# Kernel tuning notes

Measured on AMD Instinct MI355X. Metric: run time of the kernel, lower is better.

Reference implementation:

```python
import jax, jax.numpy as jnp
import numpy as np

B, D_DATA, D_DICT0, N_SAE, D_DICT = 2048, 768, 128, 128, 32


def _kaiming_uniform(key, shape, fan_in):
    # torch.nn.init.kaiming_uniform_ default: bound = sqrt(6 / fan_in) / sqrt(5-gain stuff) ~ use gain=sqrt(2)? match torch default a=sqrt(5) not needed; plain kaiming_uniform_ uses gain=sqrt(2): bound = sqrt(6/fan_in)*? Keep simple: bound = sqrt(6.0/fan_in)
    bound = np.sqrt(6.0 / fan_in)
    return jax.random.uniform(key, shape, jnp.float32, -bound, bound)


def setup_inputs() -> dict:
    key = jax.random.key(0)
    ks = jax.random.split(key, 6)
    x = jax.random.normal(ks[0], (B, D_DATA), jnp.float32)
    # top-level SAE params
    W_enc0 = _kaiming_uniform(ks[1], (D_DATA, D_DICT0), D_DATA)
    b_enc0 = jnp.zeros((D_DICT0,), jnp.float32)
    W_dec0 = _kaiming_uniform(ks[2], (D_DICT0, D_DATA), D_DICT0)
    W_dec0 = W_dec0 / jnp.linalg.norm(W_dec0, axis=-1, keepdims=True)
    b_dec0 = jnp.zeros((D_DATA,), jnp.float32)
    # sublayer (hierarchical) per-expert params
    W_enc1 = _kaiming_uniform(ks[3], (N_SAE, D_DATA, D_DICT), D_DATA)
    b_enc1 = jnp.zeros((N_SAE, D_DICT), jnp.float32)
    W_dec1 = _kaiming_uniform(ks[4], (N_SAE, D_DICT, D_DATA), D_DICT)
    W_dec1 = W_dec1 / jnp.linalg.norm(W_dec1, axis=-1, keepdims=True)
    b_dec1 = jnp.zeros((N_SAE, D_DATA), jnp.float32)
    return {"x": x, "W_enc0": W_enc0, "b_enc0": b_enc0, "W_dec0": W_dec0,
            "b_dec0": b_dec0, "W_enc1": W_enc1, "b_enc1": b_enc1,
            "W_dec1": W_dec1, "b_dec1": b_dec1}


def reference(x, W_enc0, b_enc0, W_dec0, b_dec0, W_enc1, b_enc1, W_dec1, b_dec1):
    # ---- sae_0 (standard SAE; scale/unscale are identity) ----
    acts0 = jax.nn.relu((x - b_dec0) @ W_enc0 + b_enc0)        # [B, D_DICT0]
    x0 = acts0 @ W_dec0 + b_dec0                               # [B, D_DATA]
    # ---- binary gate over experts (n_sae == d_dict0) ----
    gate = (acts0 > 0).astype(x.dtype)                         # [B, N_SAE]
    # ---- sublayer: gather-encode-decode-scatter, expressed densely with a
    # binary mask (gate only selects membership; gate value is not multiplied).
    # Avoid materializing [B, N_SAE, D_DATA] by distributing (x - b_dec1[j]):
    pre = (jnp.einsum('bd,jdk->bjk', x, W_enc1)
           - jnp.einsum('jd,jdk->jk', b_dec1, W_enc1)[None]
           + b_enc1[None])                                     # [B, N_SAE, D_DICT]
    acts1 = jax.nn.relu(pre) * gate[:, :, None]                # zero out ungated
    # scatter_add over experts: sum_j gated (acts1[b,j] @ W_dec1[j] + b_dec1[j])
    dec = jnp.einsum('bjk,jkd->bd', acts1, W_dec1) + gate @ b_dec1  # [B, D_DATA]
    return x0 + dec
```

## Files before the change

kernel.cpp:

```cpp
#include <hip/hip_runtime.h>
#include <hip/hip_bf16.h>
#include <stdint.h>

#define B_SZ   2048
#define DDATA  768
#define NSAE   128
#define NJK    4096
#define KA2    4352
#define SPLITK 4
#define KC2    1088

typedef unsigned short u16;
typedef short bf16x8 __attribute__((ext_vector_type(8)));
typedef float f32x4  __attribute__((ext_vector_type(4)));

static __device__ __forceinline__ u16 f2bf(float f) {
  __hip_bfloat16 h = __float2bfloat16(f);
  return *reinterpret_cast<u16*>(&h);
}

static __device__ __forceinline__ void gload16(const u16* g, u16* l) {
  __builtin_amdgcn_global_load_lds(
      (const __attribute__((address_space(1))) unsigned int*)g,
      (__attribute__((address_space(3))) unsigned int*)l,
      16, 0, 0);
}

__global__ __launch_bounds__(256) void k_front(const float* __restrict__ x,
                                               const float* __restrict__ We0,
                                               const float* __restrict__ be0,
                                               const float* __restrict__ bd0,
                                               const float* __restrict__ We1,
                                               const float* __restrict__ bd1,
                                               const float* __restrict__ be1,
                                               const float* __restrict__ Wd1,
                                               const float* __restrict__ Wd0,
                                               u16* __restrict__ W1T,
                                               float* __restrict__ cvp,
                                               u16* __restrict__ B2T,
                                               u16* __restrict__ xb,
                                               u16* __restrict__ A2) {
  __shared__ float smem[6280];
  const int bid = blockIdx.x, t = threadIdx.x;
  if (bid < 512) {
    const int b0 = bid * 4;
    float* xs   = smem;
    float* part = smem + 3072;
    float* wqp  = smem + 5120;
    float* xns  = smem + 5632;
#pragma unroll
    for (int i = 0; i < 3; ++i) {
      int idx = t + i * 256;
      int r = idx / 192, c4 = idx % 192;
      size_t go = (size_t)(b0 + r) * DDATA + c4 * 4;
      float4 v = *(const float4*)&x[go];
      ushort4 o;
      o.x = f2bf(v.x); o.y = f2bf(v.y); o.z = f2bf(v.z); o.w = f2bf(v.w);
      *(ushort4*)&xb[go] = o;
      float4 b4 = *(const float4*)&bd0[c4 * 4];
      v.x -= b4.x; v.y -= b4.y; v.z -= b4.z; v.w -= b4.w;
      *(float4*)&xs[r * DDATA + c4 * 4] = v;
    }
    __syncthreads();
    const int ln = t & 63, w = t >> 6;
    {
      float a = 0.f;
#pragma unroll
      for (int q = 0; q < 12; ++q) { float xv = xs[w * DDATA + ln + q * 64]; a += xv * xv; }
#pragma unroll
      for (int sh = 32; sh; sh >>= 1) a += __shfl_xor(a, sh, 64);
      if (ln == 0) xns[w] = a;
    }
    const int j0 = ln * 2;
    float a00=0.f,a01=0.f,a10=0.f,a11=0.f,a20=0.f,a21=0.f,a30=0.f,a31=0.f;
    float wq0=0.f, wq1=0.f;
    const int dbase = w * 192;
    for (int d = dbase; d < dbase + 192; d += 4) {
      float4 xv0 = *(const float4*)&xs[0 * DDATA + d];
      float4 xv1 = *(const float4*)&xs[1 * DDATA + d];
      float4 xv2 = *(const float4*)&xs[2 * DDATA + d];
      float4 xv3 = *(const float4*)&xs[3 * DDATA + d];
#pragma unroll
      for (int dd = 0; dd < 4; ++dd) {
        float2 w2 = *(const float2*)&We0[(size_t)(d + dd) * 128 + j0];
        float x0 = ((const float*)&xv0)[dd], x1 = ((const float*)&xv1)[dd];
        float x2 = ((const float*)&xv2)[dd], x3 = ((const float*)&xv3)[dd];
        a00 += x0 * w2.x; a01 += x0 * w2.y;
        a10 += x1 * w2.x; a11 += x1 * w2.y;
        a20 += x2 * w2.x; a21 += x2 * w2.y;
        a30 += x3 * w2.x; a31 += x3 * w2.y;
        wq0 += w2.x * w2.x; wq1 += w2.y * w2.y;
      }
    }
    *(float2*)&part[(w * 4 + 0) * 128 + j0] = make_float2(a00, a01);
    *(float2*)&part[(w * 4 + 1) * 128 + j0] = make_float2(a10, a11);
    *(float2*)&part[(w * 4 + 2) * 128 + j0] = make_float2(a20, a21);
    *(float2*)&part[(w * 4 + 3) * 128 + j0] = make_float2(a30, a31);
    *(float2*)&wqp[w * 128 + j0] = make_float2(wq0, wq1);
    __syncthreads();
    float p0 = be0[j0], p1 = be0[j0 + 1];
    float wn0 = 0.f, wn1 = 0.f;
#pragma unroll
    for (int q = 0; q < 4; ++q) {
      float2 pr = *(const float2*)&part[(q * 4 + w) * 128 + j0];
      p0 += pr.x; p1 += pr.y;
      float2 wr2 = *(const float2*)&wqp[q * 128 + j0];
      wn0 += wr2.x; wn1 += wr2.y;
    }
    const float sx = sqrtf(xns[w]);
    const float tau0 = 1e-4f * sx * sqrtf(wn0);
    const float tau1 = 1e-4f * sx * sqrtf(wn1);
    const int bb = b0 + w;
    const size_t row = (size_t)bb * KA2;
    unsigned pk = (unsigned)f2bf(p0 > 0.f ? p0 : 0.f) |
                  ((unsigned)f2bf(p1 > 0.f ? p1 : 0.f) << 16);
    unsigned gk = (p0 > 0.f ? 0x3F80u : 0u) | (p1 > 0.f ? 0x3F800000u : 0u);
    *(unsigned*)&A2[row + NJK + j0]       = pk;
    *(unsigned*)&A2[row + NJK + 128 + j0] = gk;
#pragma unroll
    for (int c = 0; c < 2; ++c) {
      float pv = c ? p1 : p0;
      float tv = c ? tau1 : tau0;
      unsigned long long mask = __ballot(fabsf(pv) <= tv);
      while (mask) {
        int src = (int)__builtin_ctzll(mask);
        mask &= mask - 1;
        int jj = src * 2 + c;
        double acc = 0.0;
#pragma unroll
        for (int q = 0; q < 12; ++q) {
          int d = ln + q * 64;
          acc += (double)(x[(size_t)bb * DDATA + d] - bd0[d]) *
                 (double)We0[(size_t)d * 128 + jj];
        }
#pragma unroll
        for (int sh = 32; sh; sh >>= 1) acc += __shfl_xor(acc, sh, 64);
        if (ln == src) {
          double pd = acc + (double)be0[jj];
          A2[row + NJK + jj]       = f2bf(pd > 0.0 ? (float)pd : 0.f);
          A2[row + NJK + 128 + jj] = (pd > 0.0) ? (u16)0x3F80 : (u16)0;
        }
      }
    }
  } else if (bid < 896) {
    const int e = bid - 512;
    const int j = e & 127, seg = e >> 7;
    float* ts  = smem;
    float* bds = smem + 64 * 33;
    float* red = smem + 64 * 33 + 64;
    const int k = t & 31, g = t >> 5;
    float cacc = 0.f;
    for (int db = seg * 4; db < seg * 4 + 4; ++db) {
      const float* src = We1 + (size_t)j * 24576 + db * 2048;
#pragma unroll
      for (int i = 0; i < 8; ++i) {
        int ee = t + i * 256;
        ts[(ee >> 5) * 33 + (ee & 31)] = src[ee];
      }
      if (t < 64) bds[t] = bd1[(size_t)j * DDATA + db * 64 + t];
      __syncthreads();
#pragma unroll
      for (int i = 0; i < 8; ++i) {
        int ee = t + i * 256;
        int kk = ee >> 6, d = ee & 63;
        W1T[(size_t)(j * 32 + kk) * DDATA + db * 64 + d] = f2bf(ts[d * 33 + kk]);
      }
#pragma unroll
      for (int q = 0; q < 8; ++q) {
        int d = g + 8 * q;
        cacc += ts[d * 33 + k] * bds[d];
      }
      __syncthreads();
    }
    red[g * 32 + k] = cacc;
    __syncthreads();
    if (g == 0) {
      float s = 0.f;
#pragma unroll
      for (int q = 0; q < 8; ++q) s += red[q * 32 + k];
      cvp[seg * 4096 + j * 32 + k] = (seg == 0 ? be1[j * 32 + k] : 0.f) - s;
    }
  } else {
    const int e2 = bid - 896;
    const int rb = e2 / 12, dbk = e2 % 12;
    const float* src; int r0, base;
    if (rb < 64)      { src = Wd1; r0 = rb * 64;        base = 0;    }
    else if (rb < 66) { src = Wd0; r0 = (rb - 64) * 64; base = 4096; }
    else              { src = bd1; r0 = (rb - 66) * 64; base = 4224; }
    const int d0 = dbk * 64;
#pragma unroll
    for (int i = 0; i < 16; ++i) {
      int ee = t + i * 256;
      int ri = ee >> 6, di = ee & 63;
      smem[ri * 65 + di] = src[(size_t)(r0 + ri) * DDATA + d0 + di];
    }
    __syncthreads();
#pragma unroll
    for (int i = 0; i < 16; ++i) {
      int ee = t + i * 256;
      int di = ee >> 6, ri = ee & 63;
      B2T[(size_t)(d0 + di) * KA2 + base + r0 + ri] = f2bf(smem[ri * 65 + di]);
    }
  }
}

template<int BM, int BN, int EPI>
__global__ __launch_bounds__(256) void k_gemm(const u16* __restrict__ A,
                                              const u16* __restrict__ Bm,
                                              int K, int Kc,
                                              float* __restrict__ outF,
                                              u16* __restrict__ A2,
                                              const float* __restrict__ cvec) {
  constexpr int WM = BM / 32, WN = BN / 32;
  __shared__ __align__(16) u16 As[BM * 64];
  __shared__ __align__(16) u16 Bs[BN * 64];
  __shared__ u16 gate_s[BM * 4];
  __shared__ float cv_s[BN];
  const int tid = threadIdx.x;
  int bx, by, bz;
  {
    const int h = blockIdx.x;
    if (EPI == 1) {
      const int l = (h & 7) * 128 + (h >> 3);
      const int g2 = l >> 7, w = l & 127;
      by = w >> 2; bx = (g2 << 2) + (w & 3); bz = 0;
    } else {
      const int l = (h & 7) * 192 + (h >> 3);
      bx = l >> 7; const int r2 = l & 127; bz = r2 >> 5; by = r2 & 31;
    }
  }
  const int kbase = bz * Kc;
  const u16* Ab = A  + (size_t)(by * BM) * K;
  const u16* Bb = Bm + (size_t)(bx * BN) * K;
  const int wave = tid >> 6, lane = tid & 63;
  const int wr = wave >> 1, wc = wave & 1;
  const int m0 = wr * (BM / 2), n0 = wc * (BN / 2);
  const int lm = lane & 15, qd = lane >> 4;

  if (EPI == 1) {
    for (int e = tid; e < BM * 4; e += 256) {
      int r = e >> 2, q = e & 3;
      gate_s[e] = A2[(size_t)(by * BM + r) * KA2 + NJK + 128 + bx * 4 + q];
    }
    for (int e = tid; e < BN; e += 256)
      cv_s[e] = cvec[bx * BN + e] + cvec[4096 + bx * BN + e] + cvec[8192 + bx * BN + e];
  }

  f32x4 acc[WM][WN];
  const f32x4 zero = {0.f, 0.f, 0.f, 0.f};
  for (int mi = 0; mi < WM; ++mi)
    for (int ni = 0; ni < WN; ++ni) acc[mi][ni] = zero;

  for (int k0 = kbase; k0 < kbase + Kc; k0 += 64) {
#pragma unroll
    for (int i = 0; i < BM / 32; ++i) {
      int id = tid + 256 * i;
      int row = id >> 3, u = id & 7;
      gload16(Ab + (size_t)row * K + k0 + ((u ^ (row & 7)) * 8), &As[id * 8]);
    }
#pragma unroll
    for (int i = 0; i < BN / 32; ++i) {
      int id = tid + 256 * i;
      int row = id >> 3, u = id & 7;
      gload16(Bb + (size_t)row * K + k0 + ((u ^ (row & 7)) * 8), &Bs[id * 8]);
    }
    __syncthreads();
#pragma unroll
    for (int s = 0; s < 2; ++s) {
      const int swz = ((s << 2) + qd) ^ (lm & 7);
      bf16x8 af[WM], bfv[WN];
#pragma unroll
      for (int mi = 0; mi < WM; ++mi)
        af[mi] = *(const bf16x8*)&As[(m0 + mi * 16 + lm) * 64 + swz * 8];
#pragma unroll
      for (int ni = 0; ni < WN; ++ni)
        bfv[ni] = *(const bf16x8*)&Bs[(n0 + ni * 16 + lm) * 64 + swz * 8];
#pragma unroll
      for (int mi = 0; mi < WM; ++mi)
#pragma unroll
        for (int ni = 0; ni < WN; ++ni)
          acc[mi][ni] = __builtin_amdgcn_mfma_f32_16x16x32_bf16(af[mi], bfv[ni],
                                                                acc[mi][ni], 0, 0, 0);
    }
    __syncthreads();
  }

  const int rb = qd * 4;
#pragma unroll
  for (int mi = 0; mi < WM; ++mi) {
#pragma unroll
    for (int ni = 0; ni < WN; ++ni) {
#pragma unroll
      for (int r = 0; r < 4; ++r) {
        int ml = m0 + mi * 16 + rb + r;
        int nl = n0 + ni * 16 + lm;
        int gm = by * BM + ml;
        int gn = bx * BN + nl;
        float v = acc[mi][ni][r];
        if (EPI == 1) {
          v += cv_s[nl];
          v = v > 0.f ? v : 0.f;
          u16 gbit = gate_s[ml * 4 + (nl >> 5)];
          v = gbit ? v : 0.f;
          float vn = __shfl_xor(v, 1, 64);
          if ((lm & 1) == 0) {
            unsigned pk = (unsigned)f2bf(v) | ((unsigned)f2bf(vn) << 16);
            *(unsigned*)&A2[(size_t)gm * KA2 + gn] = pk;
          }
        } else {
          outF[((size_t)bz * B_SZ + gm) * DDATA + gn] = v;
        }
      }
    }
  }
}

__global__ __launch_bounds__(256) void k_reduce(const float* __restrict__ part,
                                                const float* __restrict__ bias,
                                                float* __restrict__ out) {
  const int N4 = B_SZ * DDATA / 4;
  int i = blockIdx.x * 256 + threadIdx.x;
  const float4* p4 = (const float4*)part;
  float4 s = p4[i];
#pragma unroll
  for (int z = 1; z < SPLITK; ++z) {
    float4 t = p4[i + z * N4];
    s.x += t.x; s.y += t.y; s.z += t.z; s.w += t.w;
  }
  float4 b = ((const float4*)bias)[i % (DDATA / 4)];
  s.x += b.x; s.y += b.y; s.z += b.z; s.w += b.w;
  ((float4*)out)[i] = s;
}

extern "C" void kernel_launch(void* const* d_in, const int* in_sizes, int n_in,
                              void* d_out, int out_size, void* d_ws, size_t ws_size,
                              hipStream_t stream) {
  const float* x   = (const float*)d_in[0];
  const float* We0 = (const float*)d_in[1];
  const float* be0 = (const float*)d_in[2];
  const float* Wd0 = (const float*)d_in[3];
  const float* bd0 = (const float*)d_in[4];
  const float* We1 = (const float*)d_in[5];
  const float* be1 = (const float*)d_in[6];
  const float* Wd1 = (const float*)d_in[7];
  const float* bd1 = (const float*)d_in[8];
  float* out = (float*)d_out;

  uint8_t* ws = (uint8_t*)d_ws;
  size_t off = 0;
  auto carve = [&](size_t bytes) {
    uint8_t* p = ws + off;
    off += (bytes + 255) & ~(size_t)255;
    return p;
  };
  u16*    A2   = (u16*)carve((size_t)B_SZ * KA2 * 2);
  u16*    xb   = (u16*)carve((size_t)B_SZ * DDATA * 2);
  u16*    W1T  = (u16*)carve((size_t)NJK * DDATA * 2);
  u16*    B2T  = (u16*)carve((size_t)DDATA * KA2 * 2);
  float*  cvp  = (float*)carve((size_t)3 * NJK * 4);
  float*  part = (float*)carve((size_t)SPLITK * B_SZ * DDATA * 4);

  k_front <<<1712, 256, 0, stream>>>(x, We0, be0, bd0, We1, bd1, be1, Wd1, Wd0,
                                     W1T, cvp, B2T, xb, A2);
  k_gemm<64, 128, 1><<<1024, 256, 0, stream>>>(xb, W1T, DDATA, DDATA,
                                               nullptr, A2, cvp);
  k_gemm<64, 64, 2><<<1536, 256, 0, stream>>>(A2, B2T, KA2, KC2,
                                              part, nullptr, nullptr);
  k_reduce<<<1536, 256, 0, stream>>>(part, bd0, out);
}
```

Baseline: 167.3 us.

## Move B2T transpose into first GEMM launch and widen decode GEMM tile

New measurement: 155.8 us. 1.07x faster.

```diff
diff --git a/kernel.cpp b/kernel.cpp
--- a/kernel.cpp
+++ b/kernel.cpp
@@ -9,6 +9,7 @@
 #define KA2    4352
 #define SPLITK 4
 #define KC2    1088
+#define B2TB   816
 
 typedef unsigned short u16;
 typedef short bf16x8 __attribute__((ext_vector_type(8)));
@@ -33,11 +34,8 @@
                                                const float* __restrict__ We1,
                                                const float* __restrict__ bd1,
                                                const float* __restrict__ be1,
-                                               const float* __restrict__ Wd1,
-                                               const float* __restrict__ Wd0,
                                                u16* __restrict__ W1T,
                                                float* __restrict__ cvp,
-                                               u16* __restrict__ B2T,
                                                u16* __restrict__ xb,
                                                u16* __restrict__ A2) {
   __shared__ float smem[6280];
@@ -142,7 +140,7 @@
         }
       }
     }
-  } else if (bid < 896) {
+  } else {
     const int e = bid - 512;
     const int j = e & 127, seg = e >> 7;
     float* ts  = smem;
@@ -180,27 +178,6 @@
       for (int q = 0; q < 8; ++q) s += red[q * 32 + k];
       cvp[seg * 4096 + j * 32 + k] = (seg == 0 ? be1[j * 32 + k] : 0.f) - s;
     }
-  } else {
-    const int e2 = bid - 896;
-    const int rb = e2 / 12, dbk = e2 % 12;
-    const float* src; int r0, base;
-    if (rb < 64)      { src = Wd1; r0 = rb * 64;        base = 0;    }
-    else if (rb < 66) { src = Wd0; r0 = (rb - 64) * 64; base = 4096; }
-    else              { src = bd1; r0 = (rb - 66) * 64; base = 4224; }
-    const int d0 = dbk * 64;
-#pragma unroll
-    for (int i = 0; i < 16; ++i) {
-      int ee = t + i * 256;
-      int ri = ee >> 6, di = ee & 63;
-      smem[ri * 65 + di] = src[(size_t)(r0 + ri) * DDATA + d0 + di];
-    }
-    __syncthreads();
-#pragma unroll
-    for (int i = 0; i < 16; ++i) {
-      int ee = t + i * 256;
-      int di = ee >> 6, ri = ee & 63;
-      B2T[(size_t)(d0 + di) * KA2 + base + r0 + ri] = f2bf(smem[ri * 65 + di]);
-    }
   }
 }
 
@@ -210,24 +187,51 @@
                                               int K, int Kc,
                                               float* __restrict__ outF,
                                               u16* __restrict__ A2,
-                                              const float* __restrict__ cvec) {
+                                              const float* __restrict__ cvec,
+                                              const float* __restrict__ Wd1,
+                                              const float* __restrict__ Wd0,
+                                              const float* __restrict__ bd1,
+                                              u16* __restrict__ B2Tp) {
   constexpr int WM = BM / 32, WN = BN / 32;
-  __shared__ __align__(16) u16 As[BM * 64];
-  __shared__ __align__(16) u16 Bs[BN * 64];
+  __shared__ __align__(16) u16 AsBs[(BM + BN) * 64];
   __shared__ u16 gate_s[BM * 4];
   __shared__ float cv_s[BN];
   const int tid = threadIdx.x;
+  const int h = blockIdx.x;
+
+  if (EPI == 1 && h < B2TB) {
+    float* fsm = (float*)&AsBs[0];
+    const int rb = h / 12, dbk = h % 12;
+    const float* src; int r0, base;
+    if (rb < 64)      { src = Wd1; r0 = rb * 64;        base = 0;    }
+    else if (rb < 66) { src = Wd0; r0 = (rb - 64) * 64; base = 4096; }
+    else              { src = bd1; r0 = (rb - 66) * 64; base = 4224; }
+    const int d0 = dbk * 64;
+#pragma unroll
+    for (int i = 0; i < 16; ++i) {
+      int ee = tid + i * 256;
+      int ri = ee >> 6, di = ee & 63;
+      fsm[ri * 65 + di] = src[(size_t)(r0 + ri) * DDATA + d0 + di];
+    }
+    __syncthreads();
+#pragma unroll
+    for (int i = 0; i < 16; ++i) {
+      int ee = tid + i * 256;
+      int di = ee >> 6, ri = ee & 63;
+      B2Tp[(size_t)(d0 + di) * KA2 + base + r0 + ri] = f2bf(fsm[ri * 65 + di]);
+    }
+    return;
+  }
+
   int bx, by, bz;
-  {
-    const int h = blockIdx.x;
-    if (EPI == 1) {
-      const int l = (h & 7) * 128 + (h >> 3);
-      const int g2 = l >> 7, w = l & 127;
-      by = w >> 2; bx = (g2 << 2) + (w & 3); bz = 0;
-    } else {
-      const int l = (h & 7) * 192 + (h >> 3);
-      bx = l >> 7; const int r2 = l & 127; bz = r2 >> 5; by = r2 & 31;
-    }
+  if (EPI == 1) {
+    const int hg = h - B2TB;
+    const int l = (hg & 7) * 128 + (hg >> 3);
+    const int g2 = l >> 7, w = l & 127;
+    by = w >> 2; bx = (g2 << 2) + (w & 3); bz = 0;
+  } else {
+    const int l = (h & 7) * 96 + (h >> 3);
+    bx = l >> 7; const int r2 = l & 127; bz = r2 >> 5; by = r2 & 31;
   }
   const int kbase = bz * Kc;
   const u16* Ab = A  + (size_t)(by * BM) * K;
@@ -236,6 +240,8 @@
   const int wr = wave >> 1, wc = wave & 1;
   const int m0 = wr * (BM / 2), n0 = wc * (BN / 2);
   const int lm = lane & 15, qd = lane >> 4;
+  u16* As = &AsBs[0];
+  u16* Bs = &AsBs[BM * 64];
 
   if (EPI == 1) {
     for (int e = tid; e < BM * 4; e += 256) {
@@ -360,11 +366,11 @@
   float*  cvp  = (float*)carve((size_t)3 * NJK * 4);
   float*  part = (float*)carve((size_t)SPLITK * B_SZ * DDATA * 4);
 
-  k_front <<<1712, 256, 0, stream>>>(x, We0, be0, bd0, We1, bd1, be1, Wd1, Wd0,
-                                     W1T, cvp, B2T, xb, A2);
-  k_gemm<64, 128, 1><<<1024, 256, 0, stream>>>(xb, W1T, DDATA, DDATA,
-                                               nullptr, A2, cvp);
-  k_gemm<64, 64, 2><<<1536, 256, 0, stream>>>(A2, B2T, KA2, KC2,
-                                              part, nullptr, nullptr);
+  k_front <<<896, 256, 0, stream>>>(x, We0, be0, bd0, We1, bd1, be1,
+                                    W1T, cvp, xb, A2);
+  k_gemm<64, 128, 1><<<B2TB + 1024, 256, 0, stream>>>(
+      xb, W1T, DDATA, DDATA, nullptr, A2, cvp, Wd1, Wd0, bd1, B2T);
+  k_gemm<64, 128, 2><<<768, 256, 0, stream>>>(
+      A2, B2T, KA2, KC2, part, nullptr, nullptr, nullptr, nullptr, nullptr, nullptr);
   k_reduce<<<1536, 256, 0, stream>>>(part, bd0, out);
 }
```
